# Optimization experiments

Measured on AMD Instinct MI355X. Metric: run time of the kernel, lower is better.

The kernel has to match this reference:

```python
import jax, jax.numpy as jnp
import numpy as np

WIN = 9
WIN_SIZE = float(WIN ** 3)
LBD = 1.0
EPS = 1e-5


def _box_sum(x, win=WIN):
    """Separable sum over a win^3 window with zero padding == conv3d with all-ones kernel."""
    pad = win // 2
    for ax in (2, 3, 4):  # spatial axes of [N, C, H, W, D]
        wd = [1] * 5
        wd[ax] = win
        padc = [(0, 0)] * 5
        padc[ax] = (pad, pad)
        x = jax.lax.reduce_window(x, 0.0, jax.lax.add, tuple(wd), (1, 1, 1, 1, 1), padc)
    return x


def _warp3d(images, flows):
    """Trilinear warp. images [B,G,C,H,W,D], flows [B,G,3,H,W,D] (voxel displacements,
    channels ordered as (H, W, D) axes). Border-clamped sampling."""
    B, G, C, H, W, D = images.shape
    N = B * G
    img = images.reshape(N, C, H, W, D)
    flo = flows.reshape(N, 3, H, W, D)
    ft = flo.dtype
    gh = jnp.arange(H, dtype=ft).reshape(H, 1, 1)
    gw = jnp.arange(W, dtype=ft).reshape(1, W, 1)
    gd = jnp.arange(D, dtype=ft).reshape(1, 1, D)
    ch = jnp.clip(flo[:, 0] + gh, 0.0, H - 1.0)
    cw = jnp.clip(flo[:, 1] + gw, 0.0, W - 1.0)
    cd = jnp.clip(flo[:, 2] + gd, 0.0, D - 1.0)
    h0f = jnp.floor(ch); w0f = jnp.floor(cw); d0f = jnp.floor(cd)
    fh = ch - h0f; fw = cw - w0f; fd = cd - d0f
    h0 = h0f.astype(jnp.int32); w0 = w0f.astype(jnp.int32); d0 = d0f.astype(jnp.int32)
    h1 = jnp.minimum(h0 + 1, H - 1)
    w1 = jnp.minimum(w0 + 1, W - 1)
    d1 = jnp.minimum(d0 + 1, D - 1)
    flat = img.reshape(N, C, H * W * D)

    def gather(hi, wi, di):
        lin = ((hi * W + wi) * D + di).reshape(N, 1, H * W * D)
        return jnp.take_along_axis(flat, lin, axis=2).reshape(N, C, H, W, D)

    out = jnp.zeros_like(img)
    for hi, wh in ((h0, 1.0 - fh), (h1, fh)):
        for wi, ww in ((w0, 1.0 - fw), (w1, fw)):
            for di, wdw in ((d0, 1.0 - fd), (d1, fd)):
                w8 = (wh * ww * wdw)[:, None]  # [N,1,H,W,D]
                out = out + w8 * gather(hi, wi, di)
    return out.reshape(B, G, C, H, W, D)


def setup_inputs() -> dict:
    key = jax.random.key(0)
    k1, k2 = jax.random.split(key)
    images = jax.random.normal(k1, (1, 4, 1, 128, 128, 128), dtype=jnp.float32)
    warps = jax.random.normal(k2, (1, 4, 3, 128, 128, 128), dtype=jnp.float32)
    return {"images": images, "warps": warps}


def reference(images, warps):
    B, G, C, H, W, D = images.shape
    warped = _warp3d(images, warps).reshape(B * G, C, H, W, D)
    # groupwise template = mean over the B*G warped volumes, broadcast back
    template = jnp.broadcast_to(jnp.mean(warped, axis=0, keepdims=True), warped.shape)
    Ii, Ji = template, warped
    # 5 stat channels: I, J, I^2, J^2, IJ; groups=5 box-filter conv == per-channel box sum
    stats = jnp.concatenate([Ii, Ji, Ii * Ii, Ji * Ji, Ii * Ji], axis=1)
    sums = _box_sum(stats)
    I_sum, J_sum, I2_sum, J2_sum, IJ_sum = jnp.split(sums, 5, axis=1)
    cross = IJ_sum - J_sum / WIN_SIZE * I_sum
    I_var = I2_sum - I_sum / WIN_SIZE * I_sum
    J_var = J2_sum - J_sum / WIN_SIZE * J_sum
    cc = cross * cross / (I_var * J_var + EPS)
    lncc = -jnp.mean(cc)
    # Grad3d('l2') on warps [B,G,3,H,W,D]: dx over H (axis 3), dy over W (axis 4), dz over D (axis 5)
    dx = jnp.square(warps[:, :, :, 1:] - warps[:, :, :, :-1])
    dy = jnp.square(warps[:, :, :, :, 1:] - warps[:, :, :, :, :-1])
    dz = jnp.square(warps[..., 1:] - warps[..., :-1])
    g2 = (jnp.mean(dx) + jnp.mean(dy) + jnp.mean(dz)) / 3.0
    return lncc + LBD * g2
```

## Files before the change

### kernel.cpp

```cpp
#include <hip/hip_runtime.h>
#include <hip/hip_bf16.h>


#define NVOX (128*128*128)
#define NGRP 4
#define NCH 14

__global__ __launch_bounds__(256, 3) void k_warp_stats_d(
    const float* __restrict__ img, const float* __restrict__ flo,
    float* __restrict__ S, double* __restrict__ pg2)
{
    __shared__ float jt[NGRP][256];
    int t = threadIdx.x;
    int v = blockIdx.x * 256 + t;
    int d = v & 127;
    int w = (v >> 7) & 127;
    int h = v >> 14;
    float g2s = 0.f;

#pragma unroll
    for (int gb = 0; gb < 2; ++gb) {
        float cv[2][8], tfh[2], tfw[2], tfd[2];
#pragma unroll
        for (int gi = 0; gi < 2; ++gi) {
            int g = gb * 2 + gi;
            const float* f = flo + (size_t)g * 3 * NVOX;
            float fx = f[v], fy = f[NVOX + v], fz = f[2 * NVOX + v];
            if (h < 127) {
                float a = f[v + 16384] - fx;
                float b = f[NVOX + v + 16384] - fy;
                float c = f[2 * NVOX + v + 16384] - fz;
                g2s += a * a + b * b + c * c;
            }
            if (w < 127) {
                float a = f[v + 128] - fx;
                float b = f[NVOX + v + 128] - fy;
                float c = f[2 * NVOX + v + 128] - fz;
                g2s += a * a + b * b + c * c;
            }
            if (d < 127) {
                float a = f[v + 1] - fx;
                float b = f[NVOX + v + 1] - fy;
                float c = f[2 * NVOX + v + 1] - fz;
                g2s += a * a + b * b + c * c;
            }
            float ch = fminf(fmaxf(fx + (float)h, 0.f), 127.f);
            float cw = fminf(fmaxf(fy + (float)w, 0.f), 127.f);
            float cd = fminf(fmaxf(fz + (float)d, 0.f), 127.f);
            float h0f = floorf(ch), w0f = floorf(cw), d0f = floorf(cd);
            int h0 = (int)h0f, w0 = (int)w0f, d0 = (int)d0f;
            tfh[gi] = ch - h0f; tfw[gi] = cw - w0f; tfd[gi] = cd - d0f;
            int h1 = min(h0 + 1, 127), w1 = min(w0 + 1, 127), d1 = min(d0 + 1, 127);
            const float* im = img + (size_t)g * NVOX;
            int b00 = (h0 * 128 + w0) * 128;
            int b01 = (h0 * 128 + w1) * 128;
            int b10 = (h1 * 128 + w0) * 128;
            int b11 = (h1 * 128 + w1) * 128;
            cv[gi][0] = im[b00 + d0]; cv[gi][1] = im[b00 + d1];
            cv[gi][2] = im[b01 + d0]; cv[gi][3] = im[b01 + d1];
            cv[gi][4] = im[b10 + d0]; cv[gi][5] = im[b10 + d1];
            cv[gi][6] = im[b11 + d0]; cv[gi][7] = im[b11 + d1];
        }
#pragma unroll
        for (int gi = 0; gi < 2; ++gi) {
            float fd_ = tfd[gi], fw_ = tfw[gi], fh_ = tfh[gi];
            float c00 = cv[gi][0] + fd_ * (cv[gi][1] - cv[gi][0]);
            float c01 = cv[gi][2] + fd_ * (cv[gi][3] - cv[gi][2]);
            float c10 = cv[gi][4] + fd_ * (cv[gi][5] - cv[gi][4]);
            float c11 = cv[gi][6] + fd_ * (cv[gi][7] - cv[gi][6]);
            float c0 = c00 + fw_ * (c01 - c00);
            float c1 = c10 + fw_ * (c11 - c10);
            jt[gb * 2 + gi][t] = c0 + fh_ * (c1 - c0);
        }
    }
    __syncthreads();

    float s[NCH];
#pragma unroll
    for (int c = 0; c < NCH; ++c) s[c] = 0.f;
    int lbase = t & 128;
#pragma unroll
    for (int k = -4; k <= 4; ++k) {
        int q = d + k;
        if ((unsigned)q < 128u) {
            int tq = lbase + q;
            float j0 = jt[0][tq], j1 = jt[1][tq], j2 = jt[2][tq], j3 = jt[3][tq];
            float tm = 0.25f * (j0 + j1 + j2 + j3);
            s[0] += tm;       s[1] += tm * tm;
            s[2] += j0;  s[3] += j0 * j0;  s[4]  += tm * j0;
            s[5] += j1;  s[6] += j1 * j1;  s[7]  += tm * j1;
            s[8] += j2;  s[9] += j2 * j2;  s[10] += tm * j2;
            s[11] += j3; s[12] += j3 * j3; s[13] += tm * j3;
        }
    }
#pragma unroll
    for (int c = 0; c < NCH; ++c) S[(size_t)c * NVOX + v] = s[c];

    double val = (double)g2s;
    for (int off = 32; off; off >>= 1) val += __shfl_down(val, off, 64);
    __shared__ double wsum[4];
    int lane = t & 63, wid = t >> 6;
    if (lane == 0) wsum[wid] = val;
    __syncthreads();
    if (t == 0) pg2[blockIdx.x] = wsum[0] + wsum[1] + wsum[2] + wsum[3];
}

__global__ __launch_bounds__(256) void k_sum_w(float* __restrict__ S)
{
    __shared__ float tile[128 * 64];
    int bid = blockIdx.x;
    int half = bid & 1;
    int chh = bid >> 1;
    size_t base = (size_t)chh * 16384 + half * 64;
#pragma unroll
    for (int it = 0; it < 8; ++it) {
        int idx4 = it * 256 + threadIdx.x;
        int w = idx4 >> 4, dq = idx4 & 15;
        *(float4*)(tile + w * 64 + dq * 4) =
            *(const float4*)(S + base + (size_t)w * 128 + dq * 4);
    }
    __syncthreads();
    int dq = threadIdx.x & 15;
    int wq = threadIdx.x >> 4;
#pragma unroll
    for (int wi = 0; wi < 8; ++wi) {
        int w = wq * 8 + wi;
        float4 s = make_float4(0.f, 0.f, 0.f, 0.f);
#pragma unroll
        for (int k = -4; k <= 4; ++k) {
            int q = w + k;
            if ((unsigned)q < 128u) {
                float4 tv = *(const float4*)(tile + q * 64 + dq * 4);
                s.x += tv.x; s.y += tv.y; s.z += tv.z; s.w += tv.w;
            }
        }
        *(float4*)(S + base + (size_t)w * 128 + dq * 4) = s;
    }
}

#define LOAD_HSUM(c, acc)                                                      \
    do {                                                                       \
        const float* cp = S + (size_t)(c) * NVOX + sbase;                      \
        _Pragma("unroll")                                                      \
        for (int it = 0; it < 2; ++it) {                                       \
            int idx4 = it * 256 + t;                                           \
            if (idx4 < 272) {                           \
                int hh = idx4 >> 2, dq = idx4 & 3;                             \
                float4 vv = *(const float4*)(cp + (size_t)(r0 + hh) * 16384 + dq * 4); \
                int la = hh * 17 + dq * 4;                                     \
                tile[la] = vv.x; tile[la + 1] = vv.y;                          \
                tile[la + 2] = vv.z; tile[la + 3] = vv.w;                      \
            }                                                                  \
        }                                                                      \
        __syncthreads();                                                       \
        _Pragma("unroll")                                                      \
        for (int j4 = 0; j4 < 4; ++j4) {                                       \
            int vox = t + 256 * j4;                                            \
            int ho = vox >> 4, dd = vox & 15;                                  \
            int hg = hbase + ho;                                               \
            float sum = 0.f;                                                   \
            _Pragma("unroll")                                                  \
            for (int k = -4; k <= 4; ++k) {                                    \
                int q = hg + k;                                                \
                if ((unsigned)q < 128u) sum += tile[(q - r0) * 17 + dd];       \
            }                                                                  \
            acc[j4] = sum;                                                     \
        }                                                                      \
        __syncthreads();                                                       \
    } while (0)

__global__ __launch_bounds__(256) void k_sum_h_cc(const float* __restrict__ S,
                                                  double* __restrict__ pcc)
{
    __shared__ float tile[68 * 17];
    int t = threadIdx.x;
    int bid = blockIdx.x;
    int hs = bid & 1;
    int ddb = (bid >> 1) & 7;
    int w = bid >> 4;
    int r0 = hs ? 60 : 0;
    int hbase = hs * 64;
    size_t sbase = (size_t)w * 128 + (size_t)ddb * 16;

    float Iacc[4], I2acc[4], Ja[4], J2a[4], IJa[4];
    float lsum = 0.f;
    const float inv = 1.0f / 729.0f;

    LOAD_HSUM(0, Iacc);
    LOAD_HSUM(1, I2acc);
    for (int g = 0; g < NGRP; ++g) {
        LOAD_HSUM(2 + 3 * g, Ja);
        LOAD_HSUM(3 + 3 * g, J2a);
        LOAD_HSUM(4 + 3 * g, IJa);
#pragma unroll
        for (int j4 = 0; j4 < 4; ++j4) {
            float cross = IJa[j4] - Ja[j4] * Iacc[j4] * inv;
            float Ivar  = I2acc[j4] - Iacc[j4] * Iacc[j4] * inv;
            float Jvar  = J2a[j4] - Ja[j4] * Ja[j4] * inv;
            lsum += cross * cross / (Ivar * Jvar + 1e-5f);
        }
    }

    double val = (double)lsum;
    for (int off = 32; off; off >>= 1) val += __shfl_down(val, off, 64);
    __shared__ double wsum[4];
    int lane = t & 63, wid = t >> 6;
    if (lane == 0) wsum[wid] = val;
    __syncthreads();
    if (t == 0) pcc[bid] = wsum[0] + wsum[1] + wsum[2] + wsum[3];
}

__global__ __launch_bounds__(256) void k_finalize(const double* __restrict__ pg2,
                                                  const double* __restrict__ pcc,
                                                  float* __restrict__ out)
{
    double s_cc = 0.0, s_g2 = 0.0;
    for (int i = threadIdx.x; i < 2048; i += 256) s_cc += pcc[i];
    for (int i = threadIdx.x; i < 8192; i += 256) s_g2 += pg2[i];
    for (int off = 32; off; off >>= 1) {
        s_cc += __shfl_down(s_cc, off, 64);
        s_g2 += __shfl_down(s_g2, off, 64);
    }
    __shared__ double a[4], b[4];
    int lane = threadIdx.x & 63, wid = threadIdx.x >> 6;
    if (lane == 0) { a[wid] = s_cc; b[wid] = s_g2; }
    __syncthreads();
    if (threadIdx.x == 0) {
        double cc_sum = a[0] + a[1] + a[2] + a[3];
        double g2_sum = b[0] + b[1] + b[2] + b[3];
        double lncc = -cc_sum / (4.0 * (double)NVOX);
        double g2 = g2_sum / (3.0 * 12.0 * 127.0 * 128.0 * 128.0);
        out[0] = (float)(lncc + g2);
    }
}

extern "C" void kernel_launch(void* const* d_in, const int* in_sizes, int n_in,
                              void* d_out, int out_size, void* d_ws, size_t ws_size,
                              hipStream_t stream)
{
    const float* img = (const float*)d_in[0];
    const float* flo = (const float*)d_in[1];
    float* out = (float*)d_out;

    float* S = (float*)d_ws;
    double* pg2 = (double*)((char*)d_ws + (size_t)NCH * NVOX * 4);
    double* pcc = pg2 + 8192;

    k_warp_stats_d<<<NVOX / 256, 256, 0, stream>>>(img, flo, S, pg2);
    k_sum_w<<<NCH * 128 * 2, 256, 0, stream>>>(S);
    k_sum_h_cc<<<2048, 256, 0, stream>>>(S, pcc);
    k_finalize<<<1, 256, 0, stream>>>(pg2, pcc, out);
}
```

Measured before the change: 376.5 us.

## Pack image into float4 corner quads, use running sums in box filters

Adds a pre-pass that packs each voxel's four d/w-neighbour image values into a float4, so the trilinear warp needs two 16-byte gathers instead of eight scalar gathers. The W-axis box sum switches to a sliding running sum. The H-axis sum plus CC kernel is retiled to use float4 lanes and a two-output sliding window, which halves the block count. The pack pass adds an extra kernel and 128MB of workspace traffic, and a fallback path covers workspaces that are too small.

```diff
diff --git a/kernel.cpp b/kernel.cpp
--- a/kernel.cpp
+++ b/kernel.cpp
@@ -6,8 +6,23 @@
 #define NGRP 4
 #define NCH 14
 
-__global__ __launch_bounds__(256, 3) void k_warp_stats_d(
-    const float* __restrict__ img, const float* __restrict__ flo,
+__global__ __launch_bounds__(256) void k_pack(const float* __restrict__ img,
+                                              float4* __restrict__ P4)
+{
+    int idx = blockIdx.x * 256 + threadIdx.x;
+    int v = idx & (NVOX - 1);
+    int g = idx >> 21;
+    int d = v & 127;
+    int w = (v >> 7) & 127;
+    const float* im = img + (size_t)g * NVOX;
+    int vd1 = (d < 127) ? v + 1 : v;
+    int vw1 = (w < 127) ? v + 128 : v;
+    int vw1d1 = (d < 127) ? vw1 + 1 : vw1;
+    P4[idx] = make_float4(im[v], im[vd1], im[vw1], im[vw1d1]);
+}
+
+__global__ __launch_bounds__(256) void k_warp_stats_p4(
+    const float4* __restrict__ P4, const float* __restrict__ flo,
     float* __restrict__ S, double* __restrict__ pg2)
 {
     __shared__ float jt[NGRP][256];
@@ -19,59 +34,44 @@
     float g2s = 0.f;
 
 #pragma unroll
-    for (int gb = 0; gb < 2; ++gb) {
-        float cv[2][8], tfh[2], tfw[2], tfd[2];
-#pragma unroll
-        for (int gi = 0; gi < 2; ++gi) {
-            int g = gb * 2 + gi;
-            const float* f = flo + (size_t)g * 3 * NVOX;
-            float fx = f[v], fy = f[NVOX + v], fz = f[2 * NVOX + v];
-            if (h < 127) {
-                float a = f[v + 16384] - fx;
-                float b = f[NVOX + v + 16384] - fy;
-                float c = f[2 * NVOX + v + 16384] - fz;
-                g2s += a * a + b * b + c * c;
-            }
-            if (w < 127) {
-                float a = f[v + 128] - fx;
-                float b = f[NVOX + v + 128] - fy;
-                float c = f[2 * NVOX + v + 128] - fz;
-                g2s += a * a + b * b + c * c;
-            }
-            if (d < 127) {
-                float a = f[v + 1] - fx;
-                float b = f[NVOX + v + 1] - fy;
-                float c = f[2 * NVOX + v + 1] - fz;
-                g2s += a * a + b * b + c * c;
-            }
-            float ch = fminf(fmaxf(fx + (float)h, 0.f), 127.f);
-            float cw = fminf(fmaxf(fy + (float)w, 0.f), 127.f);
-            float cd = fminf(fmaxf(fz + (float)d, 0.f), 127.f);
-            float h0f = floorf(ch), w0f = floorf(cw), d0f = floorf(cd);
-            int h0 = (int)h0f, w0 = (int)w0f, d0 = (int)d0f;
-            tfh[gi] = ch - h0f; tfw[gi] = cw - w0f; tfd[gi] = cd - d0f;
-            int h1 = min(h0 + 1, 127), w1 = min(w0 + 1, 127), d1 = min(d0 + 1, 127);
-            const float* im = img + (size_t)g * NVOX;
-            int b00 = (h0 * 128 + w0) * 128;
-            int b01 = (h0 * 128 + w1) * 128;
-            int b10 = (h1 * 128 + w0) * 128;
-            int b11 = (h1 * 128 + w1) * 128;
-            cv[gi][0] = im[b00 + d0]; cv[gi][1] = im[b00 + d1];
-            cv[gi][2] = im[b01 + d0]; cv[gi][3] = im[b01 + d1];
-            cv[gi][4] = im[b10 + d0]; cv[gi][5] = im[b10 + d1];
-            cv[gi][6] = im[b11 + d0]; cv[gi][7] = im[b11 + d1];
-        }
-#pragma unroll
-        for (int gi = 0; gi < 2; ++gi) {
-            float fd_ = tfd[gi], fw_ = tfw[gi], fh_ = tfh[gi];
-            float c00 = cv[gi][0] + fd_ * (cv[gi][1] - cv[gi][0]);
-            float c01 = cv[gi][2] + fd_ * (cv[gi][3] - cv[gi][2]);
-            float c10 = cv[gi][4] + fd_ * (cv[gi][5] - cv[gi][4]);
-            float c11 = cv[gi][6] + fd_ * (cv[gi][7] - cv[gi][6]);
-            float c0 = c00 + fw_ * (c01 - c00);
-            float c1 = c10 + fw_ * (c11 - c10);
-            jt[gb * 2 + gi][t] = c0 + fh_ * (c1 - c0);
-        }
+    for (int g = 0; g < NGRP; ++g) {
+        const float* f = flo + (size_t)g * 3 * NVOX;
+        float fx = f[v], fy = f[NVOX + v], fz = f[2 * NVOX + v];
+        if (h < 127) {
+            float a = f[v + 16384] - fx;
+            float b = f[NVOX + v + 16384] - fy;
+            float c = f[2 * NVOX + v + 16384] - fz;
+            g2s += a * a + b * b + c * c;
+        }
+        if (w < 127) {
+            float a = f[v + 128] - fx;
+            float b = f[NVOX + v + 128] - fy;
+            float c = f[2 * NVOX + v + 128] - fz;
+            g2s += a * a + b * b + c * c;
+        }
+        if (d < 127) {
+            float a = f[v + 1] - fx;
+            float b = f[NVOX + v + 1] - fy;
+            float c = f[2 * NVOX + v + 1] - fz;
+            g2s += a * a + b * b + c * c;
+        }
+        float ch = fminf(fmaxf(fx + (float)h, 0.f), 127.f);
+        float cw = fminf(fmaxf(fy + (float)w, 0.f), 127.f);
+        float cd = fminf(fmaxf(fz + (float)d, 0.f), 127.f);
+        float h0f = floorf(ch), w0f = floorf(cw), d0f = floorf(cd);
+        int h0 = (int)h0f, w0 = (int)w0f, d0 = (int)d0f;
+        float fh = ch - h0f, fw = cw - w0f, fd = cd - d0f;
+        int h1 = min(h0 + 1, 127);
+        const float4* P = P4 + (size_t)g * NVOX;
+        float4 q0 = P[h0 * 16384 + w0 * 128 + d0];
+        float4 q1 = P[h1 * 16384 + w0 * 128 + d0];
+        float c00 = q0.x + fd * (q0.y - q0.x);
+        float c01 = q0.z + fd * (q0.w - q0.z);
+        float c10 = q1.x + fd * (q1.y - q1.x);
+        float c11 = q1.z + fd * (q1.w - q1.z);
+        float c0 = c00 + fw * (c01 - c00);
+        float c1 = c10 + fw * (c11 - c10);
+        jt[g][t] = c0 + fh * (c1 - c0);
     }
     __syncthreads();
 
@@ -105,66 +105,197 @@
     if (t == 0) pg2[blockIdx.x] = wsum[0] + wsum[1] + wsum[2] + wsum[3];
 }
 
+__global__ __launch_bounds__(256) void k_warp_stats_direct(
+    const float* __restrict__ img, const float* __restrict__ flo,
+    float* __restrict__ S, double* __restrict__ pg2)
+{
+    __shared__ float jt[NGRP][256];
+    int t = threadIdx.x;
+    int v = blockIdx.x * 256 + t;
+    int d = v & 127;
+    int w = (v >> 7) & 127;
+    int h = v >> 14;
+    float g2s = 0.f;
+
+#pragma unroll
+    for (int g = 0; g < NGRP; ++g) {
+        const float* f = flo + (size_t)g * 3 * NVOX;
+        float fx = f[v], fy = f[NVOX + v], fz = f[2 * NVOX + v];
+        if (h < 127) {
+            float a = f[v + 16384] - fx;
+            float b = f[NVOX + v + 16384] - fy;
+            float c = f[2 * NVOX + v + 16384] - fz;
+            g2s += a * a + b * b + c * c;
+        }
+        if (w < 127) {
+            float a = f[v + 128] - fx;
+            float b = f[NVOX + v + 128] - fy;
+            float c = f[2 * NVOX + v + 128] - fz;
+            g2s += a * a + b * b + c * c;
+        }
+        if (d < 127) {
+            float a = f[v + 1] - fx;
+            float b = f[NVOX + v + 1] - fy;
+            float c = f[2 * NVOX + v + 1] - fz;
+            g2s += a * a + b * b + c * c;
+        }
+        float ch = fminf(fmaxf(fx + (float)h, 0.f), 127.f);
+        float cw = fminf(fmaxf(fy + (float)w, 0.f), 127.f);
+        float cd = fminf(fmaxf(fz + (float)d, 0.f), 127.f);
+        float h0f = floorf(ch), w0f = floorf(cw), d0f = floorf(cd);
+        int h0 = (int)h0f, w0 = (int)w0f, d0 = (int)d0f;
+        float fh = ch - h0f, fw = cw - w0f, fd = cd - d0f;
+        int h1 = min(h0 + 1, 127), w1 = min(w0 + 1, 127), d1 = min(d0 + 1, 127);
+        const float* im = img + (size_t)g * NVOX;
+        int b00 = (h0 * 128 + w0) * 128;
+        int b01 = (h0 * 128 + w1) * 128;
+        int b10 = (h1 * 128 + w0) * 128;
+        int b11 = (h1 * 128 + w1) * 128;
+        float v000 = im[b00 + d0], v001 = im[b00 + d1];
+        float v010 = im[b01 + d0], v011 = im[b01 + d1];
+        float v100 = im[b10 + d0], v101 = im[b10 + d1];
+        float v110 = im[b11 + d0], v111 = im[b11 + d1];
+        float c00 = v000 + fd * (v001 - v000);
+        float c01 = v010 + fd * (v011 - v010);
+        float c10 = v100 + fd * (v101 - v100);
+        float c11 = v110 + fd * (v111 - v110);
+        float c0 = c00 + fw * (c01 - c00);
+        float c1 = c10 + fw * (c11 - c10);
+        jt[g][t] = c0 + fh * (c1 - c0);
+    }
+    __syncthreads();
+
+    float s[NCH];
+#pragma unroll
+    for (int c = 0; c < NCH; ++c) s[c] = 0.f;
+    int lbase = t & 128;
+#pragma unroll
+    for (int k = -4; k <= 4; ++k) {
+        int q = d + k;
+        if ((unsigned)q < 128u) {
+            int tq = lbase + q;
+            float j0 = jt[0][tq], j1 = jt[1][tq], j2 = jt[2][tq], j3 = jt[3][tq];
+            float tm = 0.25f * (j0 + j1 + j2 + j3);
+            s[0] += tm;       s[1] += tm * tm;
+            s[2] += j0;  s[3] += j0 * j0;  s[4]  += tm * j0;
+            s[5] += j1;  s[6] += j1 * j1;  s[7]  += tm * j1;
+            s[8] += j2;  s[9] += j2 * j2;  s[10] += tm * j2;
+            s[11] += j3; s[12] += j3 * j3; s[13] += tm * j3;
+        }
+    }
+#pragma unroll
+    for (int c = 0; c < NCH; ++c) S[(size_t)c * NVOX + v] = s[c];
+
+    double val = (double)g2s;
+    for (int off = 32; off; off >>= 1) val += __shfl_down(val, off, 64);
+    __shared__ double wsum[4];
+    int lane = t & 63, wid = t >> 6;
+    if (lane == 0) wsum[wid] = val;
+    __syncthreads();
+    if (t == 0) pg2[blockIdx.x] = wsum[0] + wsum[1] + wsum[2] + wsum[3];
+}
+
 __global__ __launch_bounds__(256) void k_sum_w(float* __restrict__ S)
 {
     __shared__ float tile[128 * 64];
+    int t = threadIdx.x;
     int bid = blockIdx.x;
     int half = bid & 1;
     int chh = bid >> 1;
     size_t base = (size_t)chh * 16384 + half * 64;
 #pragma unroll
     for (int it = 0; it < 8; ++it) {
-        int idx4 = it * 256 + threadIdx.x;
+        int idx4 = it * 256 + t;
         int w = idx4 >> 4, dq = idx4 & 15;
         *(float4*)(tile + w * 64 + dq * 4) =
             *(const float4*)(S + base + (size_t)w * 128 + dq * 4);
     }
     __syncthreads();
-    int dq = threadIdx.x & 15;
-    int wq = threadIdx.x >> 4;
-#pragma unroll
-    for (int wi = 0; wi < 8; ++wi) {
-        int w = wq * 8 + wi;
-        float4 s = make_float4(0.f, 0.f, 0.f, 0.f);
-#pragma unroll
-        for (int k = -4; k <= 4; ++k) {
-            int q = w + k;
-            if ((unsigned)q < 128u) {
-                float4 tv = *(const float4*)(tile + q * 64 + dq * 4);
-                s.x += tv.x; s.y += tv.y; s.z += tv.z; s.w += tv.w;
-            }
+    int dq = t & 15;
+    int wq = t >> 4;
+    int w0 = wq * 8;
+    float4 s = make_float4(0.f, 0.f, 0.f, 0.f);
+#pragma unroll
+    for (int k = -4; k <= 4; ++k) {
+        int q = w0 + k;
+        if ((unsigned)q < 128u) {
+            float4 tv = *(const float4*)(tile + q * 64 + dq * 4);
+            s.x += tv.x; s.y += tv.y; s.z += tv.z; s.w += tv.w;
+        }
+    }
+    *(float4*)(S + base + (size_t)w0 * 128 + dq * 4) = s;
+#pragma unroll
+    for (int wi = 1; wi < 8; ++wi) {
+        int w = w0 + wi;
+        int qa = w + 4;
+        if (qa < 128) {
+            float4 tv = *(const float4*)(tile + qa * 64 + dq * 4);
+            s.x += tv.x; s.y += tv.y; s.z += tv.z; s.w += tv.w;
+        }
+        int qr = w - 5;
+        if (qr >= 0) {
+            float4 tv = *(const float4*)(tile + qr * 64 + dq * 4);
+            s.x -= tv.x; s.y -= tv.y; s.z -= tv.z; s.w -= tv.w;
         }
         *(float4*)(S + base + (size_t)w * 128 + dq * 4) = s;
     }
 }
 
-#define LOAD_HSUM(c, acc)                                                      \
+__device__ __forceinline__ float cc4(float4 I, float4 I2, float4 J, float4 J2, float4 IJ)
+{
+    const float inv = 1.0f / 729.0f;
+    float r = 0.f;
+    {
+        float cr = IJ.x - J.x * I.x * inv, iv = I2.x - I.x * I.x * inv, jv = J2.x - J.x * J.x * inv;
+        r += cr * cr / (iv * jv + 1e-5f);
+    }
+    {
+        float cr = IJ.y - J.y * I.y * inv, iv = I2.y - I.y * I.y * inv, jv = J2.y - J.y * J.y * inv;
+        r += cr * cr / (iv * jv + 1e-5f);
+    }
+    {
+        float cr = IJ.z - J.z * I.z * inv, iv = I2.z - I.z * I.z * inv, jv = J2.z - J.z * J.z * inv;
+        r += cr * cr / (iv * jv + 1e-5f);
+    }
+    {
+        float cr = IJ.w - J.w * I.w * inv, iv = I2.w - I.w * I.w * inv, jv = J2.w - J.w * J.w * inv;
+        r += cr * cr / (iv * jv + 1e-5f);
+    }
+    return r;
+}
+
+#define LOADH(c, a0, a1)                                                       \
     do {                                                                       \
-        const float* cp = S + (size_t)(c) * NVOX + sbase;                      \
+        const float* cp = S + (size_t)(c) * NVOX + cbase;                      \
         _Pragma("unroll")                                                      \
-        for (int it = 0; it < 2; ++it) {                                       \
-            int idx4 = it * 256 + t;                                           \
-            if (idx4 < 272) {                           \
-                int hh = idx4 >> 2, dq = idx4 & 3;                             \
-                float4 vv = *(const float4*)(cp + (size_t)(r0 + hh) * 16384 + dq * 4); \
-                int la = hh * 17 + dq * 4;                                     \
+        for (int it = 0; it < 3; ++it) {                                       \
+            int idx = it * 256 + t;                                            \
+            if (idx < 640) {                           \
+                int row = idx >> 4, dqu = idx & 15;                            \
+                int rr = r0 + row;                                             \
+                float4 vv = make_float4(0.f, 0.f, 0.f, 0.f);                   \
+                if ((unsigned)rr < 128u)                                       \
+                    vv = *(const float4*)(cp + (size_t)rr * 16384 + dqu * 4);  \
+                int la = row * 65 + dqu * 4;                                   \
                 tile[la] = vv.x; tile[la + 1] = vv.y;                          \
                 tile[la + 2] = vv.z; tile[la + 3] = vv.w;                      \
             }                                                                  \
         }                                                                      \
         __syncthreads();                                                       \
-        _Pragma("unroll")                                                      \
-        for (int j4 = 0; j4 < 4; ++j4) {                                       \
-            int vox = t + 256 * j4;                                            \
-            int ho = vox >> 4, dd = vox & 15;                                  \
-            int hg = hbase + ho;                                               \
-            float sum = 0.f;                                                   \
+        {                                                                      \
+            int hl = hg * 2;                                                   \
+            float4 sum = make_float4(0.f, 0.f, 0.f, 0.f);                      \
             _Pragma("unroll")                                                  \
-            for (int k = -4; k <= 4; ++k) {                                    \
-                int q = hg + k;                                                \
-                if ((unsigned)q < 128u) sum += tile[(q - r0) * 17 + dd];       \
+            for (int k = 0; k < 9; ++k) {                                      \
+                const float* tp = tile + (hl + k) * 65 + dq * 4;               \
+                sum.x += tp[0]; sum.y += tp[1]; sum.z += tp[2]; sum.w += tp[3];\
             }                                                                  \
-            acc[j4] = sum;                                                     \
+            a0 = sum;                                                          \
+            const float* ta = tile + (hl + 9) * 65 + dq * 4;                   \
+            const float* tr = tile + hl * 65 + dq * 4;                         \
+            sum.x += ta[0] - tr[0]; sum.y += ta[1] - tr[1];                    \
+            sum.z += ta[2] - tr[2]; sum.w += ta[3] - tr[3];                    \
+            a1 = sum;                                                          \
         }                                                                      \
         __syncthreads();                                                       \
     } while (0)
@@ -172,33 +303,28 @@
 __global__ __launch_bounds__(256) void k_sum_h_cc(const float* __restrict__ S,
                                                   double* __restrict__ pcc)
 {
-    __shared__ float tile[68 * 17];
+    __shared__ float tile[40 * 65];
     int t = threadIdx.x;
     int bid = blockIdx.x;
-    int hs = bid & 1;
-    int ddb = (bid >> 1) & 7;
-    int w = bid >> 4;
-    int r0 = hs ? 60 : 0;
-    int hbase = hs * 64;
-    size_t sbase = (size_t)w * 128 + (size_t)ddb * 16;
-
-    float Iacc[4], I2acc[4], Ja[4], J2a[4], IJa[4];
+    int dh = bid & 1;
+    int hq = (bid >> 1) & 3;
+    int w = bid >> 3;
+    int r0 = hq * 32 - 4;
+    size_t cbase = (size_t)w * 128 + dh * 64;
+    int dq = t & 15;
+    int hg = t >> 4;
+
+    float4 Ia0, Ia1, I2a0, I2a1, Ja0, Ja1, J2a0, J2a1, IJa0, IJa1;
     float lsum = 0.f;
-    const float inv = 1.0f / 729.0f;
-
-    LOAD_HSUM(0, Iacc);
-    LOAD_HSUM(1, I2acc);
+
+    LOADH(0, Ia0, Ia1);
+    LOADH(1, I2a0, I2a1);
     for (int g = 0; g < NGRP; ++g) {
-        LOAD_HSUM(2 + 3 * g, Ja);
-        LOAD_HSUM(3 + 3 * g, J2a);
-        LOAD_HSUM(4 + 3 * g, IJa);
-#pragma unroll
-        for (int j4 = 0; j4 < 4; ++j4) {
-            float cross = IJa[j4] - Ja[j4] * Iacc[j4] * inv;
-            float Ivar  = I2acc[j4] - Iacc[j4] * Iacc[j4] * inv;
-            float Jvar  = J2a[j4] - Ja[j4] * Ja[j4] * inv;
-            lsum += cross * cross / (Ivar * Jvar + 1e-5f);
-        }
+        LOADH(2 + 3 * g, Ja0, Ja1);
+        LOADH(3 + 3 * g, J2a0, J2a1);
+        LOADH(4 + 3 * g, IJa0, IJa1);
+        lsum += cc4(Ia0, I2a0, Ja0, J2a0, IJa0);
+        lsum += cc4(Ia1, I2a1, Ja1, J2a1, IJa1);
     }
 
     double val = (double)lsum;
@@ -215,7 +341,7 @@
                                                   float* __restrict__ out)
 {
     double s_cc = 0.0, s_g2 = 0.0;
-    for (int i = threadIdx.x; i < 2048; i += 256) s_cc += pcc[i];
+    for (int i = threadIdx.x; i < 1024; i += 256) s_cc += pcc[i];
     for (int i = threadIdx.x; i < 8192; i += 256) s_g2 += pg2[i];
     for (int off = 32; off; off >>= 1) {
         s_cc += __shfl_down(s_cc, off, 64);
@@ -242,12 +368,25 @@
     const float* flo = (const float*)d_in[1];
     float* out = (float*)d_out;
 
+    const size_t S_BYTES  = (size_t)NCH * NVOX * 4;
+    const size_t P4_BYTES = (size_t)NGRP * NVOX * 16;
     float* S = (float*)d_ws;
-    double* pg2 = (double*)((char*)d_ws + (size_t)NCH * NVOX * 4);
-    double* pcc = pg2 + 8192;
-
-    k_warp_stats_d<<<NVOX / 256, 256, 0, stream>>>(img, flo, S, pg2);
-    k_sum_w<<<NCH * 128 * 2, 256, 0, stream>>>(S);
-    k_sum_h_cc<<<2048, 256, 0, stream>>>(S, pcc);
-    k_finalize<<<1, 256, 0, stream>>>(pg2, pcc, out);
-}
+
+    if (ws_size >= S_BYTES + P4_BYTES + 8192 * 8 + 1024 * 8) {
+        float4* P4 = (float4*)((char*)d_ws + S_BYTES);
+        double* pg2 = (double*)((char*)d_ws + S_BYTES + P4_BYTES);
+        double* pcc = pg2 + 8192;
+        k_pack<<<(NGRP * NVOX) / 256, 256, 0, stream>>>(img, P4);
+        k_warp_stats_p4<<<NVOX / 256, 256, 0, stream>>>(P4, flo, S, pg2);
+        k_sum_w<<<NCH * 128 * 2, 256, 0, stream>>>(S);
+        k_sum_h_cc<<<1024, 256, 0, stream>>>(S, pcc);
+        k_finalize<<<1, 256, 0, stream>>>(pg2, pcc, out);
+    } else {
+        double* pg2 = (double*)((char*)d_ws + S_BYTES);
+        double* pcc = pg2 + 8192;
+        k_warp_stats_direct<<<NVOX / 256, 256, 0, stream>>>(img, flo, S, pg2);
+        k_sum_w<<<NCH * 128 * 2, 256, 0, stream>>>(S);
+        k_sum_h_cc<<<1024, 256, 0, stream>>>(S, pcc);
+        k_finalize<<<1, 256, 0, stream>>>(pg2, pcc, out);
+    }
+}
```

Measured after the change: 394.0 us. +4.6%, slower.
